# Optimization experiments

Hardware: AMD Instinct MI355X
Metric: run time of the kernel (lower is better)

Reference implementation:

```python
import jax, jax.numpy as jnp
import numpy as np

B, CI, CO, F, H, W = 8, 32, 64, 4, 64, 64


def _grid(h, w):
    # channel 0 varies along W so dx = coords[0,1,0]-coords[0,0,0] is the uniform spacing
    xs = jnp.linspace(0.0, 1.0, w, dtype=jnp.float32)
    ys = jnp.linspace(0.0, 1.0, h, dtype=jnp.float32)
    gy, gx = jnp.meshgrid(ys, xs, indexing='ij')
    return jnp.stack([gx, gy], axis=-1)  # [h, w, 2]


def _trapz(x, dx, axis):
    # trapezoidal rule with uniform spacing dx along `axis`
    return dx * (x.sum(axis=axis) - 0.5 * (jnp.take(x, 0, axis=axis) + jnp.take(x, -1, axis=axis)))


def integral_2d(x, dx, dim1, dim2):
    # 2D quadrature over dims dim1 < dim2 (reduce dim2 first so dim1 index stays valid)
    return _trapz(_trapz(x, dx, dim2), dx, dim1)


def setup_inputs() -> dict:
    key = jax.random.key(0)
    k1, k2, k3 = jax.random.split(key, 3)
    fan_in_scale = 1.0 / np.sqrt(CI * 2)  # kaiming-ish init scale
    return {
        'v': jax.random.normal(k1, (B, CI, H, W), dtype=jnp.float32),
        'v_coords': _grid(H, W),
        'target_coords': _grid(H, W),
        'Wx': jax.random.normal(k2, (F, CO, CI, 2), dtype=jnp.float32) * fan_in_scale,
        'Wy': jax.random.normal(k3, (F, CO, CI, 2), dtype=jnp.float32) * fan_in_scale,
    }


def reference(v, v_coords, target_coords, Wx, Wy):
    # v: [b, i, h, w]; coords: [h, w, 2]; Wx/Wy: [f, o, i, 2]
    vp = jnp.transpose(v, (0, 2, 3, 1))                 # [b, h, w, i]
    dx = v_coords[0, 1, 0] - v_coords[0, 0, 0]
    iv = integral_2d(vp, dx, 1, 2)                      # [b, i]
    # == einsum('foid,hwd->hwfoi', Wx, target_coords) then 'hwfoi,bi->bhwfo'
    scaled = jnp.einsum('foid,bi,hwd->bhwfo', Wx, iv, target_coords, optimize=True)
    # == einsum('foid,hwd->hwfoi', Wy, v_coords) then 'hwfoi,bhwi->bhwfo'
    Wyvp = jnp.einsum('foid,hwd,bhwi->bhwfo', Wy, v_coords, vp, optimize=True)
    iw = integral_2d(Wyvp, dx, 1, 2)                    # [b, f, o]
    up = scaled + iw[:, None, None]                     # [b, h, w, f, o]
    up = up.sum(axis=3)                                 # [b, h, w, o]
    return jnp.transpose(up, (0, 3, 1, 2))              # [b, o, h, w]
```

## Files before the change

kernel.cpp:

```cpp
#include <hip/hip_runtime.h>
#include <hip/hip_bf16.h>

#define B_  8
#define CI_ 32
#define CO_ 64
#define F_  4
#define H_  64
#define W_  64

__global__ __launch_bounds__(1024) void k_reduce(
    const float* __restrict__ v, const float* __restrict__ vc,
    float* __restrict__ iv, float* __restrict__ T) {
  const int bi  = blockIdx.x;
  const int tid = threadIdx.x;
  const int h   = tid >> 4;
  const int w4  = tid & 15;

#define GW_(w) ((((w) == 0) || ((w) == W_ - 1)) ? 0.5f : 1.0f)
  const int wsc = w4 * 4;
  const float4 wg = make_float4(GW_(wsc), GW_(wsc + 1), GW_(wsc + 2), GW_(wsc + 3));
  const float cx0 = vc[2 * wsc],       cx1 = vc[2 * (wsc + 1)];
  const float cx2 = vc[2 * (wsc + 2)], cx3 = vc[2 * (wsc + 3)];
  const float cy  = vc[h * (W_ * 2) + 1];
  const float wh  = ((h == 0) || (h == H_ - 1)) ? 0.5f : 1.0f;

  float4 a = ((const float4*)(v + (size_t)bi * (H_ * W_)))[tid];

  float rs0 = a.x * wg.x + a.y * wg.y + a.z * wg.z + a.w * wg.w;
  float rs1 = a.x * wg.x * cx0 + a.y * wg.y * cx1 + a.z * wg.z * cx2 + a.w * wg.w * cx3;
  float s0 = wh * rs0;
  float s1 = wh * rs1;
  float s2 = wh * cy * rs0;

  for (int off = 32; off > 0; off >>= 1) {
    s0 += __shfl_down(s0, off, 64);
    s1 += __shfl_down(s1, off, 64);
    s2 += __shfl_down(s2, off, 64);
  }
  __shared__ float red[16][3];
  const int wave = tid >> 6;
  if ((tid & 63) == 0) {
    red[wave][0] = s0; red[wave][1] = s1; red[wave][2] = s2;
  }
  __syncthreads();
  if (tid < 16) {
    float t0 = red[tid][0], t1 = red[tid][1], t2 = red[tid][2];
    for (int off = 8; off > 0; off >>= 1) {
      t0 += __shfl_down(t0, off, 64);
      t1 += __shfl_down(t1, off, 64);
      t2 += __shfl_down(t2, off, 64);
    }
    if (tid == 0) {
      float dx = vc[2] - vc[0];
      float sc = dx * dx;
      iv[bi]        = t0 * sc;
      T[2 * bi]     = t1 * sc;
      T[2 * bi + 1] = t2 * sc;
    }
  }
}

__global__ __launch_bounds__(1024) void k_out_fused(
    const float* __restrict__ tc, const float* __restrict__ Wx,
    const float* __restrict__ Wy, const float* __restrict__ iv,
    const float* __restrict__ T, float* __restrict__ out) {
  const int bo  = blockIdx.x;
  const int tid = threadIdx.x;
  const int b   = bo >> 6;
  const int o   = bo & 63;

  __shared__ float red[2][3];
  __shared__ float bc[3];

  if (tid < CI_ * F_) {
    int i = tid & (CI_ - 1);
    int f = tid >> 5;
    float ivbi = iv[b * CI_ + i];
    float t0 = T[(b * CI_ + i) * 2];
    float t1 = T[(b * CI_ + i) * 2 + 1];
    int base = ((f * CO_ + o) * CI_ + i) * 2;
    float2 wx = *(const float2*)(Wx + base);
    float2 wy = *(const float2*)(Wy + base);
    float sx0 = wx.x * ivbi;
    float sx1 = wx.y * ivbi;
    float c   = wy.x * t0 + wy.y * t1;
    for (int off = 32; off > 0; off >>= 1) {
      sx0 += __shfl_down(sx0, off, 64);
      sx1 += __shfl_down(sx1, off, 64);
      c   += __shfl_down(c,   off, 64);
    }
    if ((tid & 63) == 0) {
      int wave = tid >> 6;
      red[wave][0] = sx0; red[wave][1] = sx1; red[wave][2] = c;
    }
  }
  __syncthreads();
  if (tid == 0) {
    bc[0] = red[0][0] + red[1][0];
    bc[1] = red[0][1] + red[1][1];
    bc[2] = red[0][2] + red[1][2];
  }
  __syncthreads();
  const float SX0 = bc[0], SX1 = bc[1], C = bc[2];

  const int p4 = tid;
  const int h  = p4 >> 4;
  const int wq = p4 & 15;
  const float4* tcp = (const float4*)(tc + (size_t)(h * W_ + wq * 4) * 2);
  float4 t0v = tcp[0];
  float4 t1v = tcp[1];

  float4 r;
  r.x = t0v.x * SX0 + t0v.y * SX1 + C;
  r.y = t0v.z * SX0 + t0v.w * SX1 + C;
  r.z = t1v.x * SX0 + t1v.y * SX1 + C;
  r.w = t1v.z * SX0 + t1v.w * SX1 + C;

  ((float4*)out)[(size_t)bo * 1024 + p4] = r;
}

extern "C" void kernel_launch(void* const* d_in, const int* in_sizes, int n_in,
                              void* d_out, int out_size, void* d_ws, size_t ws_size,
                              hipStream_t stream) {
  const float* v  = (const float*)d_in[0];
  const float* vc = (const float*)d_in[1];
  const float* tc = (const float*)d_in[2];
  const float* Wx = (const float*)d_in[3];
  const float* Wy = (const float*)d_in[4];
  float* out = (float*)d_out;

  float* iv = (float*)d_ws;
  float* T  = iv + B_ * CI_;

  k_reduce<<<B_ * CI_, 1024, 0, stream>>>(v, vc, iv, T);
  k_out_fused<<<B_ * CO_, 1024, 0, stream>>>(tc, Wx, Wy, iv, T, out);
}
```

Baseline: 68.98 us.

## Fuse reduction and output into one kernel with per-pair recomputed integrals

Measured after the change: 78.29 us. +13.5%, slower.

```diff
diff --git a/kernel.cpp b/kernel.cpp
--- a/kernel.cpp
+++ b/kernel.cpp
@@ -1,5 +1,4 @@
 #include <hip/hip_runtime.h>
-#include <hip/hip_bf16.h>
 
 #define B_  8
 #define CI_ 32
@@ -8,115 +7,119 @@
 #define H_  64
 #define W_  64
 
-__global__ __launch_bounds__(1024) void k_reduce(
+__global__ __launch_bounds__(1024) void k_fused(
     const float* __restrict__ v, const float* __restrict__ vc,
-    float* __restrict__ iv, float* __restrict__ T) {
-  const int bi  = blockIdx.x;
+    const float* __restrict__ tc, const float* __restrict__ Wx,
+    const float* __restrict__ Wy, float* __restrict__ out) {
+  const int blk = blockIdx.x;
+  const int b   = blk >> 5;
+  const int op  = blk & 31;
   const int tid = threadIdx.x;
-  const int h   = tid >> 4;
-  const int w4  = tid & 15;
 
+  __shared__ float4 wls[2][CI_];
+  __shared__ float  red[16][8];
+  __shared__ float  bc[2][4];
+
+  if (tid < 2 * CI_) {
+    const int i  = tid & (CI_ - 1);
+    const int oo = tid >> 5;
+    const int o  = op * 2 + oo;
+    float wx0 = 0.f, wx1 = 0.f, wy0 = 0.f, wy1 = 0.f;
+#pragma unroll
+    for (int f = 0; f < F_; ++f) {
+      const int base = ((f * CO_ + o) * CI_ + i) * 2;
+      float2 wx = *(const float2*)(Wx + base);
+      float2 wy = *(const float2*)(Wy + base);
+      wx0 += wx.x; wx1 += wx.y; wy0 += wy.x; wy1 += wy.y;
+    }
+    wls[oo][i] = make_float4(wx0, wx1, wy0, wy1);
+  }
+
+  const int h  = tid >> 4;
+  const int w4 = tid & 15;
 #define GW_(w) ((((w) == 0) || ((w) == W_ - 1)) ? 0.5f : 1.0f)
   const int wsc = w4 * 4;
-  const float4 wg = make_float4(GW_(wsc), GW_(wsc + 1), GW_(wsc + 2), GW_(wsc + 3));
+  const float wh = ((h == 0) || (h == H_ - 1)) ? 0.5f : 1.0f;
+  const float4 wg = make_float4(wh * GW_(wsc), wh * GW_(wsc + 1),
+                                wh * GW_(wsc + 2), wh * GW_(wsc + 3));
   const float cx0 = vc[2 * wsc],       cx1 = vc[2 * (wsc + 1)];
   const float cx2 = vc[2 * (wsc + 2)], cx3 = vc[2 * (wsc + 3)];
   const float cy  = vc[h * (W_ * 2) + 1];
-  const float wh  = ((h == 0) || (h == H_ - 1)) ? 0.5f : 1.0f;
 
-  float4 a = ((const float4*)(v + (size_t)bi * (H_ * W_)))[tid];
+  __syncthreads();
 
-  float rs0 = a.x * wg.x + a.y * wg.y + a.z * wg.z + a.w * wg.w;
-  float rs1 = a.x * wg.x * cx0 + a.y * wg.y * cx1 + a.z * wg.z * cx2 + a.w * wg.w * cx3;
-  float s0 = wh * rs0;
-  float s1 = wh * rs1;
-  float s2 = wh * cy * rs0;
+  float a00 = 0.f, a01 = 0.f, aC0 = 0.f;
+  float a10 = 0.f, a11 = 0.f, aC1 = 0.f;
+  const float4* vb = (const float4*)(v + (size_t)b * (CI_ * H_ * W_));
+#pragma unroll 8
+  for (int i = 0; i < CI_; ++i) {
+    float4 a = vb[i * 1024 + tid];
+    float t0 = a.x * wg.x, t1 = a.y * wg.y, t2 = a.z * wg.z, t3 = a.w * wg.w;
+    float rs0 = (t0 + t1) + (t2 + t3);
+    float rs1 = t0 * cx0 + t1 * cx1 + t2 * cx2 + t3 * cx3;
+    float rs2 = cy * rs0;
+    float4 wA = wls[0][i];
+    float4 wB = wls[1][i];
+    a00 += wA.x * rs0;  a01 += wA.y * rs0;  aC0 += wA.z * rs1 + wA.w * rs2;
+    a10 += wB.x * rs0;  a11 += wB.y * rs0;  aC1 += wB.z * rs1 + wB.w * rs2;
+  }
 
   for (int off = 32; off > 0; off >>= 1) {
-    s0 += __shfl_down(s0, off, 64);
-    s1 += __shfl_down(s1, off, 64);
-    s2 += __shfl_down(s2, off, 64);
+    a00 += __shfl_down(a00, off, 64);
+    a01 += __shfl_down(a01, off, 64);
+    aC0 += __shfl_down(aC0, off, 64);
+    a10 += __shfl_down(a10, off, 64);
+    a11 += __shfl_down(a11, off, 64);
+    aC1 += __shfl_down(aC1, off, 64);
   }
-  __shared__ float red[16][3];
   const int wave = tid >> 6;
   if ((tid & 63) == 0) {
-    red[wave][0] = s0; red[wave][1] = s1; red[wave][2] = s2;
+    red[wave][0] = a00; red[wave][1] = a01; red[wave][2] = aC0;
+    red[wave][3] = a10; red[wave][4] = a11; red[wave][5] = aC1;
   }
   __syncthreads();
   if (tid < 16) {
-    float t0 = red[tid][0], t1 = red[tid][1], t2 = red[tid][2];
+    float r0 = red[tid][0], r1 = red[tid][1], r2 = red[tid][2];
+    float r3 = red[tid][3], r4 = red[tid][4], r5 = red[tid][5];
     for (int off = 8; off > 0; off >>= 1) {
-      t0 += __shfl_down(t0, off, 64);
-      t1 += __shfl_down(t1, off, 64);
-      t2 += __shfl_down(t2, off, 64);
+      r0 += __shfl_down(r0, off, 64);
+      r1 += __shfl_down(r1, off, 64);
+      r2 += __shfl_down(r2, off, 64);
+      r3 += __shfl_down(r3, off, 64);
+      r4 += __shfl_down(r4, off, 64);
+      r5 += __shfl_down(r5, off, 64);
     }
     if (tid == 0) {
-      float dx = vc[2] - vc[0];
-      float sc = dx * dx;
-      iv[bi]        = t0 * sc;
-      T[2 * bi]     = t1 * sc;
-      T[2 * bi + 1] = t2 * sc;
-    }
-  }
-}
-
-__global__ __launch_bounds__(1024) void k_out_fused(
-    const float* __restrict__ tc, const float* __restrict__ Wx,
-    const float* __restrict__ Wy, const float* __restrict__ iv,
-    const float* __restrict__ T, float* __restrict__ out) {
-  const int bo  = blockIdx.x;
-  const int tid = threadIdx.x;
-  const int b   = bo >> 6;
-  const int o   = bo & 63;
-
-  __shared__ float red[2][3];
-  __shared__ float bc[3];
-
-  if (tid < CI_ * F_) {
-    int i = tid & (CI_ - 1);
-    int f = tid >> 5;
-    float ivbi = iv[b * CI_ + i];
-    float t0 = T[(b * CI_ + i) * 2];
-    float t1 = T[(b * CI_ + i) * 2 + 1];
-    int base = ((f * CO_ + o) * CI_ + i) * 2;
-    float2 wx = *(const float2*)(Wx + base);
-    float2 wy = *(const float2*)(Wy + base);
-    float sx0 = wx.x * ivbi;
-    float sx1 = wx.y * ivbi;
-    float c   = wy.x * t0 + wy.y * t1;
-    for (int off = 32; off > 0; off >>= 1) {
-      sx0 += __shfl_down(sx0, off, 64);
-      sx1 += __shfl_down(sx1, off, 64);
-      c   += __shfl_down(c,   off, 64);
-    }
-    if ((tid & 63) == 0) {
-      int wave = tid >> 6;
-      red[wave][0] = sx0; red[wave][1] = sx1; red[wave][2] = c;
+      const float dx = vc[2] - vc[0];
+      const float sc = dx * dx;
+      bc[0][0] = r0 * sc; bc[0][1] = r1 * sc; bc[0][2] = r2 * sc;
+      bc[1][0] = r3 * sc; bc[1][1] = r4 * sc; bc[1][2] = r5 * sc;
     }
   }
   __syncthreads();
-  if (tid == 0) {
-    bc[0] = red[0][0] + red[1][0];
-    bc[1] = red[0][1] + red[1][1];
-    bc[2] = red[0][2] + red[1][2];
+
+  const float4* tcp = (const float4*)(tc + (size_t)(h * W_ + wsc) * 2);
+  const float4 t0v = tcp[0];
+  const float4 t1v = tcp[1];
+
+  {
+    const float SX0 = bc[0][0], SX1 = bc[0][1], C = bc[0][2];
+    float4 r;
+    r.x = t0v.x * SX0 + t0v.y * SX1 + C;
+    r.y = t0v.z * SX0 + t0v.w * SX1 + C;
+    r.z = t1v.x * SX0 + t1v.y * SX1 + C;
+    r.w = t1v.z * SX0 + t1v.w * SX1 + C;
+    ((float4*)out)[(size_t)(b * CO_ + op * 2) * 1024 + tid] = r;
   }
-  __syncthreads();
-  const float SX0 = bc[0], SX1 = bc[1], C = bc[2];
-
-  const int p4 = tid;
-  const int h  = p4 >> 4;
-  const int wq = p4 & 15;
-  const float4* tcp = (const float4*)(tc + (size_t)(h * W_ + wq * 4) * 2);
-  float4 t0v = tcp[0];
-  float4 t1v = tcp[1];
-
-  float4 r;
-  r.x = t0v.x * SX0 + t0v.y * SX1 + C;
-  r.y = t0v.z * SX0 + t0v.w * SX1 + C;
-  r.z = t1v.x * SX0 + t1v.y * SX1 + C;
-  r.w = t1v.z * SX0 + t1v.w * SX1 + C;
-
-  ((float4*)out)[(size_t)bo * 1024 + p4] = r;
+  {
+    const float SX0 = bc[1][0], SX1 = bc[1][1], C = bc[1][2];
+    float4 r;
+    r.x = t0v.x * SX0 + t0v.y * SX1 + C;
+    r.y = t0v.z * SX0 + t0v.w * SX1 + C;
+    r.z = t1v.x * SX0 + t1v.y * SX1 + C;
+    r.w = t1v.z * SX0 + t1v.w * SX1 + C;
+    ((float4*)out)[(size_t)(b * CO_ + op * 2 + 1) * 1024 + tid] = r;
+  }
 }
 
 extern "C" void kernel_launch(void* const* d_in, const int* in_sizes, int n_in,
@@ -129,9 +132,5 @@
   const float* Wy = (const float*)d_in[4];
   float* out = (float*)d_out;
 
-  float* iv = (float*)d_ws;
-  float* T  = iv + B_ * CI_;
-
-  k_reduce<<<B_ * CI_, 1024, 0, stream>>>(v, vc, iv, T);
-  k_out_fused<<<B_ * CO_, 1024, 0, stream>>>(tc, Wx, Wy, iv, T, out);
+  k_fused<<<B_ * (CO_ / 2), 1024, 0, stream>>>(v, vc, tc, Wx, Wy, out);
 }
```
